# Kernel tuning notes

Hardware: AMD Instinct MI355X
Metric: run time of the kernel (lower is better)

The kernel has to match this reference:

```python
import jax, jax.numpy as jnp
import numpy as np
import math

N, D, C = 1024, 512, 70722
M_MARGIN = 0.4
H_SCALE = 0.333
S_SCALE = 64.0
EPS = 0.001


def setup_inputs() -> dict:
    key = jax.random.key(0)
    k1, k2, k3 = jax.random.split(key, 3)
    x = jax.random.normal(k1, (N, D), dtype=jnp.float32)
    labels = jax.random.randint(k2, (N,), 0, C, dtype=jnp.int64)
    # weights ~ N(0, 0.01) as in nn.Parameter init
    weights = 0.01 * jax.random.normal(k3, (C, D), dtype=jnp.float32)
    return {"x": x, "labels": labels, "weights": weights}


def reference(x, labels, weights):
    # world_size == 1: all-gather is identity and all labels are local.
    x_norms = jnp.maximum(jnp.linalg.norm(x, axis=1, keepdims=True), 1e-8)  # [N,1]

    norm_emb = x / jnp.maximum(jnp.linalg.norm(x, axis=1, keepdims=True), 1e-12)
    norm_w = weights / jnp.maximum(jnp.linalg.norm(weights, axis=1, keepdims=True), 1e-12)
    cosine = jnp.clip(norm_emb @ norm_w.T, -1.0, 1.0)  # [N,C]

    # AdaFace adaptive margin scaler (detached norms; t_alpha=1 -> batch stats = current stats)
    safe_norms = jax.lax.stop_gradient(jnp.clip(x_norms, 0.001, 100.0))  # [N,1]
    batch_mean = jnp.mean(safe_norms)
    batch_std = jnp.std(safe_norms, ddof=1)  # torch .std() is unbiased
    margin_scaler = jnp.clip((safe_norms - batch_mean) / (batch_std + EPS) * H_SCALE, -1.0, 1.0)  # [N,1]

    g_angular = -M_MARGIN * margin_scaler           # [N,1]
    g_add = M_MARGIN + M_MARGIN * margin_scaler     # [N,1]

    onehot = jax.nn.one_hot(labels, C, dtype=cosine.dtype)  # [N,C]

    theta = jnp.arccos(cosine)
    theta_m = jnp.clip(theta + onehot * g_angular, EPS, math.pi - EPS)
    logits = (jnp.cos(theta_m) - onehot * g_add) * S_SCALE  # [N,C]

    logp = jax.nn.log_softmax(logits, axis=-1)
    loss = -jnp.mean(jnp.take_along_axis(logp, labels[:, None], axis=1))
    return loss
```

## Files before the change

kernel.cpp:

```cpp
#include <hip/hip_runtime.h>
#include <hip/hip_bf16.h>
#include <stdint.h>

#define DIM 512
#define NROWS 1024
#define NCLS 70722
#define NCTILE 553

typedef float floatx4 __attribute__((ext_vector_type(4)));

__device__ __forceinline__ unsigned pk4_fp8(float a, float b, float c, float d) {
    unsigned v = 0;
    v = __builtin_amdgcn_cvt_pk_fp8_f32(a, b, v, false);
    v = __builtin_amdgcn_cvt_pk_fp8_f32(c, d, v, true);
    return v;
}

__device__ __forceinline__ float wave_reduce_sum(float s) {
    #pragma unroll
    for (int m = 1; m < 64; m <<= 1) s += __shfl_xor(s, m);
    return s;
}

__global__ __launch_bounds__(256) void prep_kernel(
        const float* __restrict__ x, const float* __restrict__ W,
        const int* __restrict__ labels,
        uint8_t* __restrict__ An, uint8_t* __restrict__ Wn8,
        float* __restrict__ rownorm, float* __restrict__ coslab,
        float* __restrict__ rowsum) {
    int b = blockIdx.x;
    int wv = threadIdx.x >> 6, lane = threadIdx.x & 63;
    if (b < NROWS / 4) {
        if (threadIdx.x < 4) rowsum[b * 4 + threadIdx.x] = 0.0f;
        int row = b * 4 + wv;
        int lab = labels[row];
        const float4* xs = (const float4*)(x + (size_t)row * DIM);
        const float4* ws = (const float4*)(W + (size_t)lab * DIM);
        float4 xa = xs[lane * 2], xb = xs[lane * 2 + 1];
        float4 wa = ws[lane * 2], wb = ws[lane * 2 + 1];
        float dxx = xa.x*xa.x + xa.y*xa.y + xa.z*xa.z + xa.w*xa.w
                  + xb.x*xb.x + xb.y*xb.y + xb.z*xb.z + xb.w*xb.w;
        float dww = wa.x*wa.x + wa.y*wa.y + wa.z*wa.z + wa.w*wa.w
                  + wb.x*wb.x + wb.y*wb.y + wb.z*wb.z + wb.w*wb.w;
        float dxw = xa.x*wa.x + xa.y*wa.y + xa.z*wa.z + xa.w*wa.w
                  + xb.x*wb.x + xb.y*wb.y + xb.z*wb.z + xb.w*wb.w;
        dxx = wave_reduce_sum(dxx);
        dww = wave_reduce_sum(dww);
        dxw = wave_reduce_sum(dxw);
        float norm = sqrtf(dxx);
        float s16 = 16.0f / fmaxf(norm, 1e-12f);
        uint2 p;
        p.x = pk4_fp8(xa.x*s16, xa.y*s16, xa.z*s16, xa.w*s16);
        p.y = pk4_fp8(xb.x*s16, xb.y*s16, xb.z*s16, xb.w*s16);
        *(uint2*)(An + (size_t)row * DIM + lane * 8) = p;
        if (lane == 0) {
            rownorm[row] = norm;
            coslab[row]  = dxw / (fmaxf(norm, 1e-12f) * fmaxf(sqrtf(dww), 1e-12f));
        }
    } else {
        int c = (b - NROWS / 4) * 4 + wv;
        if (c < NCLS) {
            const float4* src = (const float4*)(W + (size_t)c * DIM);
            float4 va = src[lane * 2], vb = src[lane * 2 + 1];
            float ss = va.x*va.x + va.y*va.y + va.z*va.z + va.w*va.w
                     + vb.x*vb.x + vb.y*vb.y + vb.z*vb.z + vb.w*vb.w;
            ss = wave_reduce_sum(ss);
            float s16 = 16.0f / fmaxf(sqrtf(ss), 1e-12f);
            uint2 p;
            p.x = pk4_fp8(va.x*s16, va.y*s16, va.z*s16, va.w*s16);
            p.y = pk4_fp8(vb.x*s16, vb.y*s16, vb.z*s16, vb.w*s16);
            *(uint2*)(Wn8 + (size_t)c * DIM + lane * 8) = p;
        }
    }
}

__global__ __launch_bounds__(256) void gemm5_kernel(
        const uint8_t* __restrict__ An, const uint8_t* __restrict__ Wn8,
        float* __restrict__ rowsum) {
    __shared__ uint8_t As[2][128 * 64];
    __shared__ uint8_t Bs[2][128 * 64];
    __shared__ float red[128];
    int b = blockIdx.x;
    int ctile = (b >> 6) * 8 + (b & 7);
    int mtile = (b >> 3) & 7;
    if (ctile >= NCTILE) return;
    int t = threadIdx.x, lane = t & 63, wv = t >> 6;
    if (t < 128) red[t] = 0.0f;

    int sr = lane >> 2;
    int gs = (sr & 3) ^ ((sr >> 2) & 3);
    int ck = (((lane & 3) ^ gs) * 16);
    const uint8_t* aG = An + (size_t)(mtile * 128 + wv * 16 + sr) * DIM + ck;
    int c0 = min(ctile * 128 + wv * 16 + sr,      NCLS - 1);
    int c1 = min(ctile * 128 + 64 + wv * 16 + sr, NCLS - 1);
    const uint8_t* bG0 = Wn8 + (size_t)c0 * DIM + ck;
    const uint8_t* bG1 = Wn8 + (size_t)c1 * DIM + ck;
    int wvoff = wv * 16 * 64;

    int wm = (wv >> 1) * 64, wn = (wv & 1) * 64;
    int fr = lane & 15, fq = lane >> 4;
    int fh = fq >> 1, fl = (fq & 1) * 8;

    floatx4 acc[4][4] = {};

#define GLL(gptr, lptr) __builtin_amdgcn_global_load_lds( \
        (const __attribute__((address_space(1))) unsigned int*)(gptr), \
        (__attribute__((address_space(3))) unsigned int*)(lptr), 16, 0, 0)

#define STAGE(buf, kc) do { \
        GLL(aG + (kc),                      As[buf] + wvoff); \
        GLL(aG + 64 * DIM + (kc),           As[buf] + wvoff + 64 * 64); \
        GLL(bG0 + (kc),                     Bs[buf] + wvoff); \
        GLL(bG1 + (kc),                     Bs[buf] + wvoff + 64 * 64); \
    } while (0)

#define COMPUTE_TILE(Ab, Bb) do { \
        long af[2][4], bf[2][4]; \
        _Pragma("unroll") \
        for (int mt = 0; mt < 4; ++mt) { \
            int R = wm + mt * 16 + fr; \
            int gRB = ((R & 3) ^ ((R >> 2) & 3)) * 16; \
            const uint8_t* rp = (Ab) + R * 64; \
            af[0][mt] = *(const long*)(rp + ((fh * 16) ^ gRB) + fl); \
            af[1][mt] = *(const long*)(rp + (((2 + fh) * 16) ^ gRB) + fl); \
        } \
        _Pragma("unroll") \
        for (int nt = 0; nt < 4; ++nt) { \
            int R = wn + nt * 16 + fr; \
            int gRB = ((R & 3) ^ ((R >> 2) & 3)) * 16; \
            const uint8_t* rp = (Bb) + R * 64; \
            bf[0][nt] = *(const long*)(rp + ((fh * 16) ^ gRB) + fl); \
            bf[1][nt] = *(const long*)(rp + (((2 + fh) * 16) ^ gRB) + fl); \
        } \
        _Pragma("unroll") \
        for (int s = 0; s < 2; ++s) \
            _Pragma("unroll") \
            for (int mt = 0; mt < 4; ++mt) \
                _Pragma("unroll") \
                for (int nt = 0; nt < 4; ++nt) \
                    acc[mt][nt] = __builtin_amdgcn_mfma_f32_16x16x32_fp8_fp8( \
                        af[s][mt], bf[s][nt], acc[mt][nt], 0, 0, 0); \
    } while (0)

    STAGE(0, 0);
    #pragma unroll
    for (int k = 0; k < 7; ++k) {
        STAGE((k + 1) & 1, (k + 1) * 64);
        asm volatile("s_waitcnt vmcnt(4)" ::: "memory");
        __builtin_amdgcn_s_barrier();
        COMPUTE_TILE(As[k & 1], Bs[k & 1]);
        asm volatile("" ::: "memory");
        __builtin_amdgcn_s_barrier();
    }
    asm volatile("s_waitcnt vmcnt(0)" ::: "memory");
    __builtin_amdgcn_s_barrier();
    COMPUTE_TILE(As[1], Bs[1]);

#undef GLL
#undef STAGE
#undef COMPUTE_TILE

    const float CLIPC = 0.99999950f;
    const float ISCL  = 1.0f / 256.0f;
    int colbase = ctile * 128 + wn + fr;
    #pragma unroll
    for (int mt = 0; mt < 4; ++mt) {
        #pragma unroll
        for (int reg = 0; reg < 4; ++reg) {
            float s = 0.0f;
            #pragma unroll
            for (int nt = 0; nt < 4; ++nt) {
                int col = colbase + nt * 16;
                float c = acc[mt][nt][reg] * ISCL;
                c = fminf(fmaxf(c, -CLIPC), CLIPC);
                float term = __expf(64.0f * c - 64.0f);
                s += (col < NCLS) ? term : 0.0f;
            }
            s += __shfl_xor(s, 1); s += __shfl_xor(s, 2);
            s += __shfl_xor(s, 4); s += __shfl_xor(s, 8);
            if (fr == 0) atomicAdd(&red[wm + mt * 16 + fq * 4 + reg], s);
        }
    }
    __syncthreads();
    if (t < 128) atomicAdd(rowsum + mtile * 128 + t, red[t]);
}

__global__ __launch_bounds__(1024) void finalize_kernel(
        const float* __restrict__ rowsum, const float* __restrict__ coslab,
        const float* __restrict__ rownorm, float* __restrict__ out) {
    __shared__ float sd[1024];
    int t = threadIdx.x;
    float v = fminf(fmaxf(rownorm[t], 0.001f), 100.0f);
    sd[t] = v; __syncthreads();
    for (int s = 512; s > 0; s >>= 1) { if (t < s) sd[t] += sd[t + s]; __syncthreads(); }
    float mean = sd[0] * (1.0f / 1024.0f);
    __syncthreads();
    float d = v - mean;
    sd[t] = d * d; __syncthreads();
    for (int s = 512; s > 0; s >>= 1) { if (t < s) sd[t] += sd[t + s]; __syncthreads(); }
    float stdv = sqrtf(sd[0] * (1.0f / 1023.0f));
    float ms = d / (stdv + 0.001f) * 0.333f;
    ms = fminf(fmaxf(ms, -1.0f), 1.0f);
    float g_ang = -0.4f * ms;
    float g_add =  0.4f + 0.4f * ms;
    const float CLIPC = 0.99999950f;
    const float PI = 3.14159265358979323846f;
    float cl  = fminf(fmaxf(coslab[t], -1.0f), 1.0f);
    float cne = fminf(fmaxf(cl, -CLIPC), CLIPC);
    float logit_non = 64.0f * cne;
    float theta = acosf(cl);
    float tm = fminf(fmaxf(theta + g_ang, 0.001f), PI - 0.001f);
    float logit_true = (__cosf(tm) - g_add) * 64.0f;
    float ssum = rowsum[t] - __expf(logit_non - 64.0f) + __expf(logit_true - 64.0f);
    float loss = logf(ssum) + 64.0f - logit_true;
    __syncthreads();
    sd[t] = loss; __syncthreads();
    for (int s = 512; s > 0; s >>= 1) { if (t < s) sd[t] += sd[t + s]; __syncthreads(); }
    if (t == 0) out[0] = sd[0] * (1.0f / 1024.0f);
}

extern "C" void kernel_launch(void* const* d_in, const int* in_sizes, int n_in,
                              void* d_out, int out_size, void* d_ws, size_t ws_size,
                              hipStream_t stream) {
    const float* x      = (const float*)d_in[0];
    const int*   labels = (const int*)d_in[1];
    const float* W      = (const float*)d_in[2];
    float* out = (float*)d_out;
    char* ws = (char*)d_ws;

    const size_t SZ_WN8 = 36212736;
    const size_t SZ_AN  = 524288;
    uint8_t* Wn8 = (uint8_t*)ws;
    uint8_t* An  = (uint8_t*)(ws + SZ_WN8);
    float* rownorm = (float*)(ws + SZ_WN8 + SZ_AN);
    float* rowsum  = rownorm + 1024;
    float* coslab  = rowsum + 1024;

    int wblocks = (NCLS + 3) / 4;
    prep_kernel<<<NROWS / 4 + wblocks, 256, 0, stream>>>(
        x, W, labels, An, Wn8, rownorm, coslab, rowsum);
    gemm5_kernel<<<70 * 64, 256, 0, stream>>>(An, Wn8, rowsum);
    finalize_kernel<<<1, 1024, 0, stream>>>(rowsum, coslab, rownorm, out);
}
```

Before: 288.1 us.

## Enlarge GEMM tile to 256x256 with 8 waves, 4-stage LDS ring and XCD remap

The FP8 cosine GEMM moves from 128x128 tiles with 4 waves to 256x256 tiles with 8 waves, each wave holding a 128x64 accumulator. It uses a 4-deep LDS ring with two k-steps prefetched, interleaves LDS fragment loads with MFMA quarter-blocks separated by barriers, and raises wave priority around the MFMAs. Block IDs are remapped so consecutive tiles land on the same XCD for L2 reuse. The larger tile cuts re-reads of the big W matrix and A across blocks, at the cost of far fewer blocks (1108), more registers and LDS, and many more barriers per k-step.

```diff
diff --git a/kernel.cpp b/kernel.cpp
--- a/kernel.cpp
+++ b/kernel.cpp
@@ -5,7 +5,7 @@
 #define DIM 512
 #define NROWS 1024
 #define NCLS 70722
-#define NCTILE 553
+#define NCT2 277
 
 typedef float floatx4 __attribute__((ext_vector_type(4)));
 
@@ -74,115 +74,151 @@
     }
 }
 
-__global__ __launch_bounds__(256) void gemm5_kernel(
+__global__ __launch_bounds__(512, 2) void gemm5_kernel(
         const uint8_t* __restrict__ An, const uint8_t* __restrict__ Wn8,
         float* __restrict__ rowsum) {
-    __shared__ uint8_t As[2][128 * 64];
-    __shared__ uint8_t Bs[2][128 * 64];
-    __shared__ float red[128];
-    int b = blockIdx.x;
-    int ctile = (b >> 6) * 8 + (b & 7);
-    int mtile = (b >> 3) & 7;
-    if (ctile >= NCTILE) return;
-    int t = threadIdx.x, lane = t & 63, wv = t >> 6;
-    if (t < 128) red[t] = 0.0f;
+    __shared__ uint8_t As[4][16384];
+    __shared__ uint8_t Bs[4][16384];
+    __shared__ float red[256];
+
+    int orig = blockIdx.x;
+    int xcd = orig & 7, idx = orig >> 3;
+    const int q = (4 * NCT2) >> 3, r = (4 * NCT2) & 7;
+    int wgid = (xcd < r ? xcd * (q + 1) : r * (q + 1) + (xcd - r) * q) + idx;
+    int mtile = wgid & 3, ctile = wgid >> 2;
+
+    int tid = threadIdx.x, lane = tid & 63, wv = tid >> 6;
+    if (tid < 256) red[tid] = 0.0f;
 
     int sr = lane >> 2;
-    int gs = (sr & 3) ^ ((sr >> 2) & 3);
-    int ck = (((lane & 3) ^ gs) * 16);
-    const uint8_t* aG = An + (size_t)(mtile * 128 + wv * 16 + sr) * DIM + ck;
-    int c0 = min(ctile * 128 + wv * 16 + sr,      NCLS - 1);
-    int c1 = min(ctile * 128 + 64 + wv * 16 + sr, NCLS - 1);
-    const uint8_t* bG0 = Wn8 + (size_t)c0 * DIM + ck;
-    const uint8_t* bG1 = Wn8 + (size_t)c1 * DIM + ck;
-    int wvoff = wv * 16 * 64;
-
-    int wm = (wv >> 1) * 64, wn = (wv & 1) * 64;
+    int gsw = (sr & 3) ^ ((sr >> 2) & 3);
+    int ck = ((lane & 3) ^ gsw) * 16;
+    const uint8_t* aG0 = An + (size_t)(mtile * 256 +       wv * 16 + sr) * DIM + ck;
+    const uint8_t* aG1 = An + (size_t)(mtile * 256 + 128 + wv * 16 + sr) * DIM + ck;
+    int cb0 = min(ctile * 256 +       wv * 16 + sr, NCLS - 1);
+    int cb1 = min(ctile * 256 + 128 + wv * 16 + sr, NCLS - 1);
+    const uint8_t* bG0 = Wn8 + (size_t)cb0 * DIM + ck;
+    const uint8_t* bG1 = Wn8 + (size_t)cb1 * DIM + ck;
+
+    int wm = (wv >> 2) * 128, wn = (wv & 3) * 64;
     int fr = lane & 15, fq = lane >> 4;
     int fh = fq >> 1, fl = (fq & 1) * 8;
-
-    floatx4 acc[4][4] = {};
-
-#define GLL(gptr, lptr) __builtin_amdgcn_global_load_lds( \
-        (const __attribute__((address_space(1))) unsigned int*)(gptr), \
-        (__attribute__((address_space(3))) unsigned int*)(lptr), 16, 0, 0)
-
-#define STAGE(buf, kc) do { \
-        GLL(aG + (kc),                      As[buf] + wvoff); \
-        GLL(aG + 64 * DIM + (kc),           As[buf] + wvoff + 64 * 64); \
-        GLL(bG0 + (kc),                     Bs[buf] + wvoff); \
-        GLL(bG1 + (kc),                     Bs[buf] + wvoff + 64 * 64); \
+    int gf = ((fr & 3) ^ ((fr >> 2) & 3)) * 16;
+    int offS0 = fr * 64 + ((fh * 16) ^ gf) + fl;
+    int offS1 = fr * 64 + (((2 + fh) * 16) ^ gf) + fl;
+
+    long af[8][2], bf[4][2];
+    floatx4 acc[8][4] = {};
+
+#define GLL(gp, lp) __builtin_amdgcn_global_load_lds( \
+        (const __attribute__((address_space(1))) unsigned int*)(gp), \
+        (__attribute__((address_space(3))) unsigned int*)(lp), 16, 0, 0)
+
+#define STAGE(tt) do { \
+        uint8_t* _al = &As[(tt) & 3][0] + wv * 1024; \
+        uint8_t* _bl = &Bs[(tt) & 3][0] + wv * 1024; \
+        int _kc = (tt) * 64; \
+        GLL(aG0 + _kc, _al); \
+        GLL(aG1 + _kc, _al + 8192); \
+        GLL(bG0 + _kc, _bl); \
+        GLL(bG1 + _kc, _bl + 8192); \
     } while (0)
 
-#define COMPUTE_TILE(Ab, Bb) do { \
-        long af[2][4], bf[2][4]; \
-        _Pragma("unroll") \
-        for (int mt = 0; mt < 4; ++mt) { \
-            int R = wm + mt * 16 + fr; \
-            int gRB = ((R & 3) ^ ((R >> 2) & 3)) * 16; \
-            const uint8_t* rp = (Ab) + R * 64; \
-            af[0][mt] = *(const long*)(rp + ((fh * 16) ^ gRB) + fl); \
-            af[1][mt] = *(const long*)(rp + (((2 + fh) * 16) ^ gRB) + fl); \
-        } \
-        _Pragma("unroll") \
-        for (int nt = 0; nt < 4; ++nt) { \
-            int R = wn + nt * 16 + fr; \
-            int gRB = ((R & 3) ^ ((R >> 2) & 3)) * 16; \
-            const uint8_t* rp = (Bb) + R * 64; \
-            bf[0][nt] = *(const long*)(rp + ((fh * 16) ^ gRB) + fl); \
-            bf[1][nt] = *(const long*)(rp + (((2 + fh) * 16) ^ gRB) + fl); \
-        } \
+#define MFMA16(mlo, nlo) do { \
         _Pragma("unroll") \
         for (int s = 0; s < 2; ++s) \
             _Pragma("unroll") \
-            for (int mt = 0; mt < 4; ++mt) \
+            for (int m = 0; m < 4; ++m) \
                 _Pragma("unroll") \
-                for (int nt = 0; nt < 4; ++nt) \
-                    acc[mt][nt] = __builtin_amdgcn_mfma_f32_16x16x32_fp8_fp8( \
-                        af[s][mt], bf[s][nt], acc[mt][nt], 0, 0, 0); \
+                for (int n = 0; n < 2; ++n) \
+                    acc[(mlo) + m][(nlo) + n] = \
+                        __builtin_amdgcn_mfma_f32_16x16x32_fp8_fp8( \
+                            af[(mlo) + m][s], bf[(nlo) + n][s], \
+                            acc[(mlo) + m][(nlo) + n], 0, 0, 0); \
     } while (0)
 
-    STAGE(0, 0);
+#define FENCE asm volatile("" ::: "memory")
+#define BAR   __builtin_amdgcn_s_barrier()
+#define PRIO1 __builtin_amdgcn_s_setprio(1)
+#define PRIO0 __builtin_amdgcn_s_setprio(0)
+
+    STAGE(0);
+    STAGE(1);
+    asm volatile("s_waitcnt vmcnt(4)" ::: "memory");
+    BAR;
+
     #pragma unroll
-    for (int k = 0; k < 7; ++k) {
-        STAGE((k + 1) & 1, (k + 1) * 64);
-        asm volatile("s_waitcnt vmcnt(4)" ::: "memory");
-        __builtin_amdgcn_s_barrier();
-        COMPUTE_TILE(As[k & 1], Bs[k & 1]);
-        asm volatile("" ::: "memory");
-        __builtin_amdgcn_s_barrier();
+    for (int kt = 0; kt < 8; ++kt) {
+        const uint8_t* Ab = &As[kt & 3][0];
+        const uint8_t* Bb = &Bs[kt & 3][0];
+        if (kt + 2 < 8) STAGE(kt + 2);
+        #pragma unroll
+        for (int m = 0; m < 4; ++m) {
+            af[m][0] = *(const long*)(Ab + (wm + m * 16) * 64 + offS0);
+            af[m][1] = *(const long*)(Ab + (wm + m * 16) * 64 + offS1);
+        }
+        #pragma unroll
+        for (int n = 0; n < 2; ++n) {
+            bf[n][0] = *(const long*)(Bb + (wn + n * 16) * 64 + offS0);
+            bf[n][1] = *(const long*)(Bb + (wn + n * 16) * 64 + offS1);
+        }
+        FENCE; BAR;
+        PRIO1; MFMA16(0, 0); PRIO0;
+        FENCE; BAR;
+        #pragma unroll
+        for (int m = 4; m < 8; ++m) {
+            af[m][0] = *(const long*)(Ab + (wm + m * 16) * 64 + offS0);
+            af[m][1] = *(const long*)(Ab + (wm + m * 16) * 64 + offS1);
+        }
+        FENCE; BAR;
+        PRIO1; MFMA16(4, 0); PRIO0;
+        FENCE; BAR;
+        #pragma unroll
+        for (int n = 2; n < 4; ++n) {
+            bf[n][0] = *(const long*)(Bb + (wn + n * 16) * 64 + offS0);
+            bf[n][1] = *(const long*)(Bb + (wn + n * 16) * 64 + offS1);
+        }
+        FENCE; BAR;
+        PRIO1; MFMA16(0, 2); PRIO0;
+        FENCE; BAR;
+        if (kt < 6)       asm volatile("s_waitcnt vmcnt(4)" ::: "memory");
+        else if (kt == 6) asm volatile("s_waitcnt vmcnt(0)" ::: "memory");
+        BAR;
+        PRIO1; MFMA16(4, 2); PRIO0;
+        FENCE; BAR;
     }
-    asm volatile("s_waitcnt vmcnt(0)" ::: "memory");
-    __builtin_amdgcn_s_barrier();
-    COMPUTE_TILE(As[1], Bs[1]);
 
 #undef GLL
 #undef STAGE
-#undef COMPUTE_TILE
+#undef MFMA16
+#undef FENCE
+#undef BAR
+#undef PRIO1
+#undef PRIO0
 
     const float CLIPC = 0.99999950f;
     const float ISCL  = 1.0f / 256.0f;
-    int colbase = ctile * 128 + wn + fr;
+    int colbase = ctile * 256 + wn + fr;
     #pragma unroll
-    for (int mt = 0; mt < 4; ++mt) {
+    for (int m = 0; m < 8; ++m) {
         #pragma unroll
         for (int reg = 0; reg < 4; ++reg) {
             float s = 0.0f;
             #pragma unroll
-            for (int nt = 0; nt < 4; ++nt) {
-                int col = colbase + nt * 16;
-                float c = acc[mt][nt][reg] * ISCL;
+            for (int n = 0; n < 4; ++n) {
+                int col = colbase + n * 16;
+                float c = acc[m][n][reg] * ISCL;
                 c = fminf(fmaxf(c, -CLIPC), CLIPC);
                 float term = __expf(64.0f * c - 64.0f);
                 s += (col < NCLS) ? term : 0.0f;
             }
             s += __shfl_xor(s, 1); s += __shfl_xor(s, 2);
             s += __shfl_xor(s, 4); s += __shfl_xor(s, 8);
-            if (fr == 0) atomicAdd(&red[wm + mt * 16 + fq * 4 + reg], s);
+            if (fr == 0) atomicAdd(&red[wm + m * 16 + fq * 4 + reg], s);
         }
     }
     __syncthreads();
-    if (t < 128) atomicAdd(rowsum + mtile * 128 + t, red[t]);
+    if (tid < 256) atomicAdd(rowsum + mtile * 256 + tid, red[tid]);
 }
 
 __global__ __launch_bounds__(1024) void finalize_kernel(
@@ -239,6 +275,6 @@
     int wblocks = (NCLS + 3) / 4;
     prep_kernel<<<NROWS / 4 + wblocks, 256, 0, stream>>>(
         x, W, labels, An, Wn8, rownorm, coslab, rowsum);
-    gemm5_kernel<<<70 * 64, 256, 0, stream>>>(An, Wn8, rowsum);
+    gemm5_kernel<<<4 * NCT2, 512, 0, stream>>>(An, Wn8, rowsum);
     finalize_kernel<<<1, 1024, 0, stream>>>(rowsum, coslab, rownorm, out);
 }
```

After: 316.7 us. +9.9%, slower.

## Make FP8 GEMM persistent with whole-K A tile resident in LDS

Applied to the files above, without the earlier changes.

Replaces the 128x128 per-tile GEMM grid with a persistent launch of 256 blocks of 512 threads. Each block loads its 128-row A slice (full K=512) into shared memory once, then loops over 256-wide class tiles with a double-buffered B pipeline over 128-byte K chunks. The intent is to stop re-fetching A for every class tile, amortise launch and prologue cost, and use larger tiles for more MFMA work per barrier. In exchange each block needs about 128KB of LDS, which limits occupancy to one block per CU. The exp/rowsum epilogue is also serialised inside the loop rather than overlapped by other blocks.

```diff
diff --git a/kernel.cpp b/kernel.cpp
--- a/kernel.cpp
+++ b/kernel.cpp
@@ -5,7 +5,6 @@
 #define DIM 512
 #define NROWS 1024
 #define NCLS 70722
-#define NCTILE 553
 
 typedef float floatx4 __attribute__((ext_vector_type(4)));
 
@@ -74,115 +73,164 @@
     }
 }
 
-__global__ __launch_bounds__(256) void gemm5_kernel(
+__global__ __launch_bounds__(512, 2) void gemm6_kernel(
         const uint8_t* __restrict__ An, const uint8_t* __restrict__ Wn8,
         float* __restrict__ rowsum) {
-    __shared__ uint8_t As[2][128 * 64];
-    __shared__ uint8_t Bs[2][128 * 64];
+    __shared__ uint8_t Asm[128 * 512];
+    __shared__ uint8_t Bsm[2][256 * 128];
     __shared__ float red[128];
+
     int b = blockIdx.x;
-    int ctile = (b >> 6) * 8 + (b & 7);
-    int mtile = (b >> 3) & 7;
-    if (ctile >= NCTILE) return;
-    int t = threadIdx.x, lane = t & 63, wv = t >> 6;
-    if (t < 128) red[t] = 0.0f;
-
-    int sr = lane >> 2;
-    int gs = (sr & 3) ^ ((sr >> 2) & 3);
-    int ck = (((lane & 3) ^ gs) * 16);
-    const uint8_t* aG = An + (size_t)(mtile * 128 + wv * 16 + sr) * DIM + ck;
-    int c0 = min(ctile * 128 + wv * 16 + sr,      NCLS - 1);
-    int c1 = min(ctile * 128 + 64 + wv * 16 + sr, NCLS - 1);
-    const uint8_t* bG0 = Wn8 + (size_t)c0 * DIM + ck;
-    const uint8_t* bG1 = Wn8 + (size_t)c1 * DIM + ck;
-    int wvoff = wv * 16 * 64;
-
-    int wm = (wv >> 1) * 64, wn = (wv & 1) * 64;
+    int mgrp = b >> 5, cgrp = b & 31;
+    int tid = threadIdx.x, lane = tid & 63, wv = tid >> 6;
+    if (tid < 128) red[tid] = 0.0f;
+
+    int arow = tid >> 5;
+    int aq = ((tid & 31) ^ (arow & 7)) * 16;
+    const uint8_t* aGb = An + (size_t)(mgrp * 128 + arow) * DIM + aq;
+
+    int brow = lane >> 3;
+    int ckB = ((lane & 7) ^ brow) * 16;
+
+    int wm = (wv >> 2) * 64, wn = (wv & 3) * 64;
     int fr = lane & 15, fq = lane >> 4;
     int fh = fq >> 1, fl = (fq & 1) * 8;
 
+    const floatx4 vzero = {0.0f, 0.0f, 0.0f, 0.0f};
     floatx4 acc[4][4] = {};
 
-#define GLL(gptr, lptr) __builtin_amdgcn_global_load_lds( \
-        (const __attribute__((address_space(1))) unsigned int*)(gptr), \
-        (__attribute__((address_space(3))) unsigned int*)(lptr), 16, 0, 0)
-
-#define STAGE(buf, kc) do { \
-        GLL(aG + (kc),                      As[buf] + wvoff); \
-        GLL(aG + 64 * DIM + (kc),           As[buf] + wvoff + 64 * 64); \
-        GLL(bG0 + (kc),                     Bs[buf] + wvoff); \
-        GLL(bG1 + (kc),                     Bs[buf] + wvoff + 64 * 64); \
-    } while (0)
-
-#define COMPUTE_TILE(Ab, Bb) do { \
-        long af[2][4], bf[2][4]; \
+#define GLL(gp, lp) __builtin_amdgcn_global_load_lds( \
+        (const __attribute__((address_space(1))) unsigned int*)(gp), \
+        (__attribute__((address_space(3))) unsigned int*)(lp), 16, 0, 0)
+#define BAR  __builtin_amdgcn_s_barrier()
+#define FEN  asm volatile("" ::: "memory")
+
+    #pragma unroll
+    for (int i = 0; i < 8; ++i)
+        GLL(aGb + i * 8192, Asm + i * 8192 + wv * 1024);
+
+    const uint8_t *bp0, *bp1, *bp2, *bp3;
+    {
+        int cb = cgrp * 256 + wv * 32 + brow;
+        bp0 = Wn8 + (size_t)min(cb,      NCLS - 1) * DIM + ckB;
+        bp1 = Wn8 + (size_t)min(cb + 8,  NCLS - 1) * DIM + ckB;
+        bp2 = Wn8 + (size_t)min(cb + 16, NCLS - 1) * DIM + ckB;
+        bp3 = Wn8 + (size_t)min(cb + 24, NCLS - 1) * DIM + ckB;
+    }
+
+#define STAGE_B(slot, kb) do { \
+        uint8_t* _d = Bsm[slot] + wv * 4096; \
+        GLL(bp0 + (kb), _d); \
+        GLL(bp1 + (kb), _d + 1024); \
+        GLL(bp2 + (kb), _d + 2048); \
+        GLL(bp3 + (kb), _d + 3072); } while (0)
+
+#define COMPUTE(slot, cA) do { \
+        long af[4][4], bg[4][4]; \
         _Pragma("unroll") \
-        for (int mt = 0; mt < 4; ++mt) { \
-            int R = wm + mt * 16 + fr; \
-            int gRB = ((R & 3) ^ ((R >> 2) & 3)) * 16; \
-            const uint8_t* rp = (Ab) + R * 64; \
-            af[0][mt] = *(const long*)(rp + ((fh * 16) ^ gRB) + fl); \
-            af[1][mt] = *(const long*)(rp + (((2 + fh) * 16) ^ gRB) + fl); \
+        for (int m = 0; m < 4; ++m) { \
+            int R = wm + m * 16 + fr; \
+            const uint8_t* rp = Asm + R * 512 + fl; \
+            _Pragma("unroll") \
+            for (int ks = 0; ks < 4; ++ks) { \
+                int cch = (cA) + ks * 2 + fh; \
+                af[m][ks] = *(const long*)(rp + ((cch ^ (R & 7)) * 16)); \
+            } \
         } \
         _Pragma("unroll") \
-        for (int nt = 0; nt < 4; ++nt) { \
-            int R = wn + nt * 16 + fr; \
-            int gRB = ((R & 3) ^ ((R >> 2) & 3)) * 16; \
-            const uint8_t* rp = (Bb) + R * 64; \
-            bf[0][nt] = *(const long*)(rp + ((fh * 16) ^ gRB) + fl); \
-            bf[1][nt] = *(const long*)(rp + (((2 + fh) * 16) ^ gRB) + fl); \
+        for (int n = 0; n < 4; ++n) { \
+            int R = wn + n * 16 + fr; \
+            const uint8_t* rp = Bsm[slot] + R * 128 + fl; \
+            _Pragma("unroll") \
+            for (int ks = 0; ks < 4; ++ks) { \
+                int cch = ks * 2 + fh; \
+                bg[n][ks] = *(const long*)(rp + ((cch ^ (R & 7)) * 16)); \
+            } \
         } \
         _Pragma("unroll") \
-        for (int s = 0; s < 2; ++s) \
+        for (int ks = 0; ks < 4; ++ks) \
             _Pragma("unroll") \
-            for (int mt = 0; mt < 4; ++mt) \
+            for (int m = 0; m < 4; ++m) \
                 _Pragma("unroll") \
-                for (int nt = 0; nt < 4; ++nt) \
-                    acc[mt][nt] = __builtin_amdgcn_mfma_f32_16x16x32_fp8_fp8( \
-                        af[s][mt], bf[s][nt], acc[mt][nt], 0, 0, 0); \
+                for (int n = 0; n < 4; ++n) \
+                    acc[m][n] = __builtin_amdgcn_mfma_f32_16x16x32_fp8_fp8( \
+                        af[m][ks], bg[n][ks], acc[m][n], 0, 0, 0); \
     } while (0)
 
-    STAGE(0, 0);
-    #pragma unroll
-    for (int k = 0; k < 7; ++k) {
-        STAGE((k + 1) & 1, (k + 1) * 64);
+    STAGE_B(0, 0);
+
+    int nct = (cgrp < 21) ? 9 : 8;
+    int c = cgrp;
+    for (int ct = 0; ct < nct; ++ct) {
+        STAGE_B(1, 128);
         asm volatile("s_waitcnt vmcnt(4)" ::: "memory");
-        __builtin_amdgcn_s_barrier();
-        COMPUTE_TILE(As[k & 1], Bs[k & 1]);
-        asm volatile("" ::: "memory");
-        __builtin_amdgcn_s_barrier();
+        BAR;
+        COMPUTE(0, 0);
+        FEN; BAR;
+        STAGE_B(0, 256);
+        asm volatile("s_waitcnt vmcnt(4)" ::: "memory");
+        BAR;
+        COMPUTE(1, 8);
+        FEN; BAR;
+        STAGE_B(1, 384);
+        asm volatile("s_waitcnt vmcnt(4)" ::: "memory");
+        BAR;
+        COMPUTE(0, 16);
+        FEN; BAR;
+        if (ct != nct - 1) {
+            int cb = (c + 32) * 256 + wv * 32 + brow;
+            bp0 = Wn8 + (size_t)min(cb,      NCLS - 1) * DIM + ckB;
+            bp1 = Wn8 + (size_t)min(cb + 8,  NCLS - 1) * DIM + ckB;
+            bp2 = Wn8 + (size_t)min(cb + 16, NCLS - 1) * DIM + ckB;
+            bp3 = Wn8 + (size_t)min(cb + 24, NCLS - 1) * DIM + ckB;
+            STAGE_B(0, 0);
+            asm volatile("s_waitcnt vmcnt(4)" ::: "memory");
+        } else {
+            asm volatile("s_waitcnt vmcnt(0)" ::: "memory");
+        }
+        BAR;
+        COMPUTE(1, 24);
+        FEN; BAR;
+
+        {
+            const float CLIPC = 0.99999950f;
+            const float ISCL  = 1.0f / 256.0f;
+            int colbase = c * 256 + wn + fr;
+            #pragma unroll
+            for (int m = 0; m < 4; ++m) {
+                #pragma unroll
+                for (int reg = 0; reg < 4; ++reg) {
+                    float s = 0.0f;
+                    #pragma unroll
+                    for (int n = 0; n < 4; ++n) {
+                        int col = colbase + n * 16;
+                        float cc = acc[m][n][reg] * ISCL;
+                        cc = fminf(fmaxf(cc, -CLIPC), CLIPC);
+                        float term = __expf(64.0f * cc - 64.0f);
+                        s += (col < NCLS) ? term : 0.0f;
+                    }
+                    s += __shfl_xor(s, 1); s += __shfl_xor(s, 2);
+                    s += __shfl_xor(s, 4); s += __shfl_xor(s, 8);
+                    if (fr == 0) atomicAdd(&red[wm + m * 16 + fq * 4 + reg], s);
+                }
+            }
+            #pragma unroll
+            for (int m = 0; m < 4; ++m)
+                #pragma unroll
+                for (int n = 0; n < 4; ++n)
+                    acc[m][n] = vzero;
+        }
+        c += 32;
     }
-    asm volatile("s_waitcnt vmcnt(0)" ::: "memory");
-    __builtin_amdgcn_s_barrier();
-    COMPUTE_TILE(As[1], Bs[1]);
 
 #undef GLL
-#undef STAGE
-#undef COMPUTE_TILE
-
-    const float CLIPC = 0.99999950f;
-    const float ISCL  = 1.0f / 256.0f;
-    int colbase = ctile * 128 + wn + fr;
-    #pragma unroll
-    for (int mt = 0; mt < 4; ++mt) {
-        #pragma unroll
-        for (int reg = 0; reg < 4; ++reg) {
-            float s = 0.0f;
-            #pragma unroll
-            for (int nt = 0; nt < 4; ++nt) {
-                int col = colbase + nt * 16;
-                float c = acc[mt][nt][reg] * ISCL;
-                c = fminf(fmaxf(c, -CLIPC), CLIPC);
-                float term = __expf(64.0f * c - 64.0f);
-                s += (col < NCLS) ? term : 0.0f;
-            }
-            s += __shfl_xor(s, 1); s += __shfl_xor(s, 2);
-            s += __shfl_xor(s, 4); s += __shfl_xor(s, 8);
-            if (fr == 0) atomicAdd(&red[wm + mt * 16 + fq * 4 + reg], s);
-        }
-    }
+#undef STAGE_B
+#undef COMPUTE
+#undef BAR
+#undef FEN
+
     __syncthreads();
-    if (t < 128) atomicAdd(rowsum + mtile * 128 + t, red[t]);
+    if (tid < 128) atomicAdd(rowsum + mgrp * 128 + tid, red[tid]);
 }
 
 __global__ __launch_bounds__(1024) void finalize_kernel(
@@ -239,6 +287,6 @@
     int wblocks = (NCLS + 3) / 4;
     prep_kernel<<<NROWS / 4 + wblocks, 256, 0, stream>>>(
         x, W, labels, An, Wn8, rownorm, coslab, rowsum);
-    gemm5_kernel<<<70 * 64, 256, 0, stream>>>(An, Wn8, rowsum);
+    gemm6_kernel<<<256, 512, 0, stream>>>(An, Wn8, rowsum);
     finalize_kernel<<<1, 1024, 0, stream>>>(rowsum, coslab, rownorm, out);
 }
```

Measured after the change: 299.3 us. 1.04x slower.
